# Performance work log

Hardware: AMD Instinct MI355X
Metric: run time of the kernel (lower is better)

The kernel has to match this reference:

```python
import jax, jax.numpy as jnp
import numpy as np

N_GLIMPSES = 3
GS = 64          # glimpse_size
IN_C = 3         # input_channels
B, H, W = 64, 512, 512


def get_glimpses(image, loc):
    """Multi-scale glimpse extraction (tf.image.extract_glimpse, centered+normalized)
    followed by antialiased bicubic resize to GS x GS, concatenated on channels."""
    b, h, w, c = image.shape
    max_size = GS * 2 ** (N_GLIMPSES - 1)
    padded = jnp.pad(image, ((0, 0), (max_size, max_size), (max_size, max_size), (0, 0)))
    hp, wp = h + 2 * max_size, w + 2 * max_size
    # normalized+centered offsets: (-1,-1)=upper-left, (1,1)=lower-right of padded image
    center = (loc + 1.0) * 0.5 * jnp.array([hp, wp], dtype=jnp.float32)  # (y, x) per batch
    glimpses = []
    for i in range(N_GLIMPSES):
        s = GS * 2 ** i  # current crop size (python int, static)
        tl = jnp.round(center - 0.5 * s).astype(jnp.int32)
        tl = jnp.clip(tl, 0, jnp.array([hp - s, wp - s], dtype=jnp.int32))

        def slice_one(img, yx):
            return jax.lax.dynamic_slice(img, (yx[0], yx[1], 0), (s, s, c))

        g = jax.vmap(slice_one)(padded, tl)                      # [B, s, s, C]
        g = jax.image.resize(g, (b, GS, GS, c), method='cubic')  # antialiased bicubic
        glimpses.append(g)
    return jnp.concatenate(glimpses, axis=-1)  # [B, GS, GS, N_GLIMPSES*C]


def setup_inputs() -> dict:
    key = jax.random.key(0)
    ks = jax.random.split(key, 10)
    image = jax.random.uniform(ks[0], (B, H, W, IN_C), dtype=jnp.float32)
    loc = jax.random.uniform(ks[1], (B, 2), dtype=jnp.float32, minval=-1.0, maxval=1.0)
    cg = N_GLIMPSES * IN_C
    # conv1_g: full-kernel (GS x GS) valid conv -> 1x1x128
    Wg = jax.random.normal(ks[2], (GS, GS, cg, 128), dtype=jnp.float32) * (1.0 / np.sqrt(GS * GS * cg))
    bg = jnp.zeros((128,), jnp.float32)
    # conv1_l: 1x1 conv on loc [B,1,1,2]
    Wl = jax.random.normal(ks[3], (2, 128), dtype=jnp.float32) * (1.0 / np.sqrt(2.0))
    bl = jnp.zeros((128,), jnp.float32)
    # out: 1x1 conv 128 -> 256
    Wo = jax.random.normal(ks[4], (128, 256), dtype=jnp.float32) * (1.0 / np.sqrt(128.0))
    bo = jnp.zeros((256,), jnp.float32)
    return {"image": image, "loc": loc, "Wg": Wg, "bg": bg, "Wl": Wl, "bl": bl, "Wo": Wo, "bo": bo}


def reference(image, loc, Wg, bg, Wl, bl, Wo, bo):
    glimpses = get_glimpses(image, loc)  # [B, GS, GS, N_GLIMPSES*IN_C]
    # conv1_g with kernel == glimpse size and VALID padding == dense contraction over hwc
    x1 = jax.nn.relu(jnp.einsum('bhwc,hwck->bk', glimpses, Wg) + bg)  # [B,128]
    x2 = jax.nn.relu(loc @ Wl + bl)                                   # [B,128]
    out = jax.nn.relu((x1 + x2) @ Wo + bo)                            # [B,256]
    return out
```

## Files before the change

kernel.cpp:

```cpp
#include <hip/hip_runtime.h>

#define IMG_H 512
#define IMG_W 512
#define PAD   256
#define HP    1024
#define BATCH 64
#define KTOT  36864
#define KTILE 144
#define KB    16
#define NTILES 256

__device__ __forceinline__ float keys_cubic(float x) {
  if (x >= 2.0f) return 0.0f;
  if (x >= 1.0f) return ((-0.5f * x + 2.5f) * x - 4.0f) * x + 2.0f;
  return ((1.5f * x - 2.5f) * x) * x + 1.0f;
}

__device__ __forceinline__ int iclamp(int v, int lo, int hi) {
  return min(max(v, lo), hi);
}

__global__ __launch_bounds__(256) void glimpse_kernel(
    const float* __restrict__ img, const float* __restrict__ loc,
    float* __restrict__ G) {
  __shared__ float tmp1[384];
  __shared__ float tmp2[768];
  const int y   = blockIdx.x & 63;
  const int b   = blockIdx.x >> 6;
  const int tid = threadIdx.x;

  const float cy = (loc[2 * b] + 1.0f) * 0.5f * 1024.0f;
  const float cx = (loc[2 * b + 1] + 1.0f) * 0.5f * 1024.0f;
  const int tly0 = iclamp((int)rintf(cy - 32.0f), 0, HP - 64);
  const int tlx0 = iclamp((int)rintf(cx - 32.0f), 0, HP - 64);
  const int tly1 = iclamp((int)rintf(cy - 64.0f), 0, HP - 128);
  const int tlx1 = iclamp((int)rintf(cx - 64.0f), 0, HP - 128);
  const int tly2 = iclamp((int)rintf(cy - 128.0f), 0, HP - 256);
  const int tlx2 = iclamp((int)rintf(cx - 128.0f), 0, HP - 256);
  const float* imb  = img + (size_t)b * (IMG_H * IMG_W * 3);
  float*       Grow = G + ((size_t)b * 64 + y) * (64 * 9);

  if (tid < 192) {
    int x = tid / 3, c = tid - 3 * (tid / 3);
    int py = tly0 + y - PAD, px = tlx0 + x - PAD;
    float v = 0.0f;
    if ((unsigned)py < (unsigned)IMG_H && (unsigned)px < (unsigned)IMG_W)
      v = imb[(py * IMG_W + px) * 3 + c];
    Grow[x * 9 + c] = v;
  }

  float wy1[8];
  int iy0_1;
  {
    float sy = ((float)y + 0.5f) * 2.0f - 0.5f;
    iy0_1 = (int)ceilf(sy - 4.0f);
    float ws = 0.0f;
#pragma unroll
    for (int t = 0; t < 8; ++t) {
      int i = iy0_1 + t;
      float w = (i >= 0 && i < 128) ? keys_cubic(fabsf(sy - (float)i) * 0.5f) : 0.0f;
      wy1[t] = w;
      ws += w;
    }
    float wi = 1.0f / ws;
#pragma unroll
    for (int t = 0; t < 8; ++t) wy1[t] *= wi;
  }
  float wy2[16];
  int iy0_2;
  {
    float sy = ((float)y + 0.5f) * 4.0f - 0.5f;
    iy0_2 = (int)ceilf(sy - 8.0f);
    float ws = 0.0f;
#pragma unroll
    for (int t = 0; t < 16; ++t) {
      int i = iy0_2 + t;
      float w = (i >= 0 && i < 256) ? keys_cubic(fabsf(sy - (float)i) * 0.25f) : 0.0f;
      wy2[t] = w;
      ws += w;
    }
    float wi = 1.0f / ws;
#pragma unroll
    for (int t = 0; t < 16; ++t) wy2[t] *= wi;
  }

  for (int e = tid; e < 384; e += 256) {
    int x = e / 3, c = e - 3 * (e / 3);
    int px = tlx1 - PAD + x;
    float a = 0.0f;
    if ((unsigned)px < (unsigned)IMG_W) {
      const float* colp = imb + (px * 3 + c);
#pragma unroll
      for (int t = 0; t < 8; ++t) {
        int py = tly1 + iy0_1 + t - PAD;
        if ((unsigned)py < (unsigned)IMG_H)
          a = fmaf(wy1[t], colp[py * (IMG_W * 3)], a);
      }
    }
    tmp1[e] = a;
  }
  for (int e = tid; e < 768; e += 256) {
    int x = e / 3, c = e - 3 * (e / 3);
    int px = tlx2 - PAD + x;
    float a = 0.0f;
    if ((unsigned)px < (unsigned)IMG_W) {
      const float* colp = imb + (px * 3 + c);
#pragma unroll
      for (int t = 0; t < 16; ++t) {
        int py = tly2 + iy0_2 + t - PAD;
        if ((unsigned)py < (unsigned)IMG_H)
          a = fmaf(wy2[t], colp[py * (IMG_W * 3)], a);
      }
    }
    tmp2[e] = a;
  }
  __syncthreads();

  for (int o = tid; o < 384; o += 256) {
    int oo = (o >= 192) ? o - 192 : o;
    int xo = oo / 3, c = oo - 3 * xo;
    if (o < 192) {
      float sx  = ((float)xo + 0.5f) * 2.0f - 0.5f;
      int   ix0 = (int)ceilf(sx - 4.0f);
      float a = 0.0f, wsx = 0.0f;
#pragma unroll
      for (int t = 0; t < 8; ++t) {
        int i = ix0 + t;
        if (i >= 0 && i < 128) {
          float w = keys_cubic(fabsf(sx - (float)i) * 0.5f);
          wsx += w;
          a = fmaf(w, tmp1[i * 3 + c], a);
        }
      }
      Grow[xo * 9 + 3 + c] = a / wsx;
    } else {
      float sx  = ((float)xo + 0.5f) * 4.0f - 0.5f;
      int   ix0 = (int)ceilf(sx - 8.0f);
      float a = 0.0f, wsx = 0.0f;
#pragma unroll
      for (int t = 0; t < 16; ++t) {
        int i = ix0 + t;
        if (i >= 0 && i < 256) {
          float w = keys_cubic(fabsf(sx - (float)i) * 0.25f);
          wsx += w;
          a = fmaf(w, tmp2[i * 3 + c], a);
        }
      }
      Grow[xo * 9 + 6 + c] = a / wsx;
    }
  }
}

__global__ __launch_bounds__(256) void gemm_kernel(
    const float* __restrict__ G, const float* __restrict__ Wg,
    float* __restrict__ partials) {
  const int tile = blockIdx.x;
  const int tid  = threadIdx.x;
  const int tn   = tid & 15;
  const int tm   = tid >> 4;
  __shared__ float Gs[2][KB][64];
  __shared__ float Ws[2][KB][128];

  const int gb = tid >> 2;
  const int gj = (tid & 3) * 4;
  const int wr = tid >> 4;
  const int wc = (tid & 15) * 8;
  const size_t gbase = (size_t)gb * KTOT + (size_t)tile * KTILE + gj;
  const size_t wbase = ((size_t)tile * KTILE + wr) * 128 + wc;

  float4 g4 = *(const float4*)(G + gbase);
  float4 wa = *(const float4*)(Wg + wbase);
  float4 wb = *(const float4*)(Wg + wbase + 4);

  float acc[4][8];
#pragma unroll
  for (int mi = 0; mi < 4; ++mi)
#pragma unroll
    for (int ni = 0; ni < 8; ++ni) acc[mi][ni] = 0.0f;

  constexpr int NCHUNK = KTILE / KB;
#pragma unroll
  for (int chunk = 0; chunk < NCHUNK; ++chunk) {
    const int buf = chunk & 1;
    Gs[buf][gj + 0][gb] = g4.x;
    Gs[buf][gj + 1][gb] = g4.y;
    Gs[buf][gj + 2][gb] = g4.z;
    Gs[buf][gj + 3][gb] = g4.w;
    *(float4*)&Ws[buf][wr][wc]     = wa;
    *(float4*)&Ws[buf][wr][wc + 4] = wb;
    __syncthreads();
    if (chunk + 1 < NCHUNK) {
      g4 = *(const float4*)(G + gbase + (chunk + 1) * KB);
      wa = *(const float4*)(Wg + wbase + (size_t)(chunk + 1) * KB * 128);
      wb = *(const float4*)(Wg + wbase + (size_t)(chunk + 1) * KB * 128 + 4);
    }
#pragma unroll
    for (int j = 0; j < KB; ++j) {
      float4 gv = *(const float4*)&Gs[buf][j][tm * 4];
      float4 w0 = *(const float4*)&Ws[buf][j][tn * 8];
      float4 w1 = *(const float4*)&Ws[buf][j][tn * 8 + 4];
      float gm[4] = {gv.x, gv.y, gv.z, gv.w};
      float wn[8] = {w0.x, w0.y, w0.z, w0.w, w1.x, w1.y, w1.z, w1.w};
#pragma unroll
      for (int mi = 0; mi < 4; ++mi)
#pragma unroll
        for (int ni = 0; ni < 8; ++ni)
          acc[mi][ni] = fmaf(gm[mi], wn[ni], acc[mi][ni]);
    }
  }

#pragma unroll
  for (int mi = 0; mi < 4; ++mi) {
    int m = tm * 4 + mi;
    float* dst = partials + ((size_t)m * NTILES + tile) * 128 + tn * 8;
    *(float4*)dst       = make_float4(acc[mi][0], acc[mi][1], acc[mi][2], acc[mi][3]);
    *(float4*)(dst + 4) = make_float4(acc[mi][4], acc[mi][5], acc[mi][6], acc[mi][7]);
  }
}

__global__ __launch_bounds__(256) void finalize_kernel(
    const float* __restrict__ partials, const float* __restrict__ loc,
    const float* __restrict__ bg, const float* __restrict__ Wl,
    const float* __restrict__ bl, const float* __restrict__ Wo,
    const float* __restrict__ bo, float* __restrict__ out) {
  const int b   = blockIdx.x;
  const int tid = threadIdx.x;

  const float4* base = (const float4*)(partials + (size_t)b * NTILES * 128);
  float4 acc = make_float4(0.f, 0.f, 0.f, 0.f);
#pragma unroll 8
  for (int i = 0; i < 32; ++i) {
    float4 v = base[(size_t)i * 256 + tid];
    acc.x += v.x; acc.y += v.y; acc.z += v.z; acc.w += v.w;
  }

  __shared__ float red[8][128];
  __shared__ float h[128];
  {
    float* r = &red[tid >> 5][(tid & 31) * 4];
    r[0] = acc.x; r[1] = acc.y; r[2] = acc.z; r[3] = acc.w;
  }
  __syncthreads();
  if (tid < 128) {
    float ss = 0.0f;
#pragma unroll
    for (int g = 0; g < 8; ++g) ss += red[g][tid];
    float x1 = fmaxf(ss + bg[tid], 0.0f);
    float x2 = fmaxf(fmaf(loc[2 * b], Wl[tid],
                          fmaf(loc[2 * b + 1], Wl[128 + tid], bl[tid])),
                     0.0f);
    h[tid] = x1 + x2;
  }
  __syncthreads();
  {
    int n = tid;
    float a = bo[n];
#pragma unroll 8
    for (int kk = 0; kk < 128; ++kk) a = fmaf(h[kk], Wo[kk * 256 + n], a);
    out[(size_t)b * 256 + n] = fmaxf(a, 0.0f);
  }
}

extern "C" void kernel_launch(void* const* d_in, const int* in_sizes, int n_in,
                              void* d_out, int out_size, void* d_ws, size_t ws_size,
                              hipStream_t stream) {
  const float* img = (const float*)d_in[0];
  const float* loc = (const float*)d_in[1];
  const float* Wg  = (const float*)d_in[2];
  const float* bg  = (const float*)d_in[3];
  const float* Wl  = (const float*)d_in[4];
  const float* bl  = (const float*)d_in[5];
  const float* Wo  = (const float*)d_in[6];
  const float* bo  = (const float*)d_in[7];
  float* out = (float*)d_out;

  float* ws = (float*)d_ws;
  float* G        = ws;
  float* partials = ws + 2359296;

  glimpse_kernel<<<BATCH * 64, 256, 0, stream>>>(img, loc, G);
  gemm_kernel<<<NTILES, 256, 0, stream>>>(G, Wg, partials);
  finalize_kernel<<<BATCH, 256, 0, stream>>>(partials, loc, bg, Wl, bl, Wo, bo, out);
}
```

Before: 318.8 us.

## Rewrite glimpse and GEMM kernels with bf16 MFMA and precomputed cubic weights

The glimpse kernel now handles 16-row strips per block, split by scale. Each block reads image rows once and accumulates vertical taps in registers, using compile-time normalized bicubic weights in place of per-pixel weight evaluation. The glimpse buffer is stored in bf16, and the GEMM now uses bf16 MFMA 16x16x32 instructions with Wg converted on the fly, which cuts memory traffic and ALU work. The trade-off is reduced precision (bf16 operands) and uncoalesced strided Wg loads in the GEMM.

```diff
diff --git a/kernel.cpp b/kernel.cpp
--- a/kernel.cpp
+++ b/kernel.cpp
@@ -1,4 +1,5 @@
 #include <hip/hip_runtime.h>
+#include <hip/hip_bf16.h>
 
 #define IMG_H 512
 #define IMG_W 512
@@ -6,216 +7,284 @@
 #define HP    1024
 #define BATCH 64
 #define KTOT  36864
-#define KTILE 144
-#define KB    16
-#define NTILES 256
-
-__device__ __forceinline__ float keys_cubic(float x) {
-  if (x >= 2.0f) return 0.0f;
-  if (x >= 1.0f) return ((-0.5f * x + 2.5f) * x - 4.0f) * x + 2.0f;
-  return ((1.5f * x - 2.5f) * x) * x + 1.0f;
-}
-
-__device__ __forceinline__ int iclamp(int v, int lo, int hi) {
-  return min(max(v, lo), hi);
+#define KTILE 192
+#define NTILES 192
+
+typedef __attribute__((ext_vector_type(8))) short short8;
+typedef __attribute__((ext_vector_type(4))) float f32x4;
+
+constexpr float keysc(float a) {
+  return a >= 2.0f ? 0.0f
+       : a >= 1.0f ? ((-0.5f * a + 2.5f) * a - 4.0f) * a + 2.0f
+       : (1.5f * a - 2.5f) * a * a + 1.0f;
+}
+constexpr float fabsc(float x) { return x < 0.f ? -x : x; }
+constexpr float K2c(int t) { return keysc(fabsc(7.5f - (float)t) * 0.25f); }
+constexpr float K1c(int t) { return keysc(fabsc(3.5f - (float)t) * 0.5f); }
+constexpr float C2 = K2c(0)+K2c(1)+K2c(2)+K2c(3)+K2c(4)+K2c(5)+K2c(6)+K2c(7)
+                    +K2c(8)+K2c(9)+K2c(10)+K2c(11)+K2c(12)+K2c(13)+K2c(14)+K2c(15);
+constexpr float C1 = K1c(0)+K1c(1)+K1c(2)+K1c(3)+K1c(4)+K1c(5)+K1c(6)+K1c(7);
+__device__ constexpr float KN2[16] = {
+  K2c(0)/C2, K2c(1)/C2, K2c(2)/C2, K2c(3)/C2, K2c(4)/C2, K2c(5)/C2, K2c(6)/C2, K2c(7)/C2,
+  K2c(8)/C2, K2c(9)/C2, K2c(10)/C2, K2c(11)/C2, K2c(12)/C2, K2c(13)/C2, K2c(14)/C2, K2c(15)/C2};
+__device__ constexpr float KN1[8] = {
+  K1c(0)/C1, K1c(1)/C1, K1c(2)/C1, K1c(3)/C1, K1c(4)/C1, K1c(5)/C1, K1c(6)/C1, K1c(7)/C1};
+
+__device__ __forceinline__ float enorm2(int o) {
+  if (o >= 2 && o <= 61) return 1.0f;
+  float s = 0.f;
+#pragma unroll
+  for (int t = 0; t < 16; ++t) { int i = 4 * o - 6 + t; if ((unsigned)i < 256u) s += KN2[t]; }
+  return 1.0f / s;
+}
+__device__ __forceinline__ float enorm1(int o) {
+  if (o >= 2 && o <= 61) return 1.0f;
+  float s = 0.f;
+#pragma unroll
+  for (int t = 0; t < 8; ++t) { int i = 2 * o - 3 + t; if ((unsigned)i < 128u) s += KN1[t]; }
+  return 1.0f / s;
+}
+
+__device__ __forceinline__ int iclamp(int v, int lo, int hi) { return min(max(v, lo), hi); }
+__device__ __forceinline__ unsigned short f2bits(float f) {
+  __hip_bfloat16 h = __float2bfloat16(f);
+  unsigned short s;
+  __builtin_memcpy(&s, &h, 2);
+  return s;
 }
 
 __global__ __launch_bounds__(256) void glimpse_kernel(
     const float* __restrict__ img, const float* __restrict__ loc,
-    float* __restrict__ G) {
-  __shared__ float tmp1[384];
-  __shared__ float tmp2[768];
-  const int y   = blockIdx.x & 63;
-  const int b   = blockIdx.x >> 6;
+    unsigned short* __restrict__ G) {
+  __shared__ __align__(16) float smem[16 * 768 + 16];
+  float* tmp = smem;
+  float* vn  = smem + 16 * 768;
+
+  const int blk = blockIdx.x;
+  const int b   = blk / 12;
+  const int r12 = blk - 12 * b;
   const int tid = threadIdx.x;
 
   const float cy = (loc[2 * b] + 1.0f) * 0.5f * 1024.0f;
   const float cx = (loc[2 * b + 1] + 1.0f) * 0.5f * 1024.0f;
-  const int tly0 = iclamp((int)rintf(cy - 32.0f), 0, HP - 64);
-  const int tlx0 = iclamp((int)rintf(cx - 32.0f), 0, HP - 64);
-  const int tly1 = iclamp((int)rintf(cy - 64.0f), 0, HP - 128);
-  const int tlx1 = iclamp((int)rintf(cx - 64.0f), 0, HP - 128);
-  const int tly2 = iclamp((int)rintf(cy - 128.0f), 0, HP - 256);
-  const int tlx2 = iclamp((int)rintf(cx - 128.0f), 0, HP - 256);
-  const float* imb  = img + (size_t)b * (IMG_H * IMG_W * 3);
-  float*       Grow = G + ((size_t)b * 64 + y) * (64 * 9);
-
-  if (tid < 192) {
-    int x = tid / 3, c = tid - 3 * (tid / 3);
-    int py = tly0 + y - PAD, px = tlx0 + x - PAD;
-    float v = 0.0f;
-    if ((unsigned)py < (unsigned)IMG_H && (unsigned)px < (unsigned)IMG_W)
-      v = imb[(py * IMG_W + px) * 3 + c];
-    Grow[x * 9 + c] = v;
-  }
-
-  float wy1[8];
-  int iy0_1;
+  const float* imb = img + (size_t)b * (IMG_H * IMG_W * 3);
+
+  if (r12 >= 8) {
+    const int y0 = 16 * (r12 - 8);
+    const int tly0 = iclamp((int)rintf(cy - 32.0f), 0, HP - 64);
+    const int tlx0 = iclamp((int)rintf(cx - 32.0f), 0, HP - 64);
+#pragma unroll
+    for (int p = 0; p < 12; ++p) {
+      int oi = tid + 256 * p;
+      int yl = oi / 192, rem = oi - 192 * yl, x = rem / 3, c = rem - 3 * x;
+      int py = tly0 + y0 + yl - PAD, px = tlx0 + x - PAD;
+      float v = 0.0f;
+      if ((unsigned)py < (unsigned)IMG_H && (unsigned)px < (unsigned)IMG_W)
+        v = imb[(py * IMG_W + px) * 3 + c];
+      G[(((size_t)b * 64 + y0 + yl) * 64 + x) * 9 + c] = f2bits(v);
+    }
+    return;
+  }
+
+  if (r12 < 4) {
+    const int y0 = 16 * r12;
+    const int tly = iclamp((int)rintf(cy - 128.0f), 0, HP - 256);
+    const int tlx = iclamp((int)rintf(cx - 128.0f), 0, HP - 256);
+    const int cb = (tlx - PAD) * 3;
+    const int xA = tid / 3, xB = (tid + 256) / 3, xC = (tid + 512) / 3;
+    const bool mA = (unsigned)(tlx - PAD + xA) < (unsigned)IMG_W;
+    const bool mB = (unsigned)(tlx - PAD + xB) < (unsigned)IMG_W;
+    const bool mC = (unsigned)(tlx - PAD + xC) < (unsigned)IMG_W;
+    float a0[16], a1[16], a2[16];
+#pragma unroll
+    for (int i = 0; i < 16; ++i) { a0[i] = 0.f; a1[i] = 0.f; a2[i] = 0.f; }
+    const int rbase = 4 * y0 - 6;
+#pragma unroll
+    for (int k = 0; k < 76; ++k) {
+      const int r = rbase + k;
+      const int py = tly - PAD + r;
+      if ((unsigned)r < 256u && (unsigned)py < (unsigned)IMG_H) {
+        const float* rp = imb + (size_t)py * (IMG_W * 3) + cb;
+        float v0 = mA ? rp[tid] : 0.f;
+        float v1 = mB ? rp[tid + 256] : 0.f;
+        float v2 = mC ? rp[tid + 512] : 0.f;
+#pragma unroll
+        for (int d = 0; d < 4; ++d) {
+          const int yl = (k >> 2) - d;
+          const int t  = (k & 3) + 4 * d;
+          if (yl >= 0 && yl < 16) {
+            const float w = KN2[t];
+            a0[yl] = fmaf(w, v0, a0[yl]);
+            a1[yl] = fmaf(w, v1, a1[yl]);
+            a2[yl] = fmaf(w, v2, a2[yl]);
+          }
+        }
+      }
+    }
+#pragma unroll
+    for (int yl = 0; yl < 16; ++yl) {
+      tmp[yl * 768 + tid]       = a0[yl];
+      tmp[yl * 768 + tid + 256] = a1[yl];
+      tmp[yl * 768 + tid + 512] = a2[yl];
+    }
+    if (tid < 16) vn[tid] = enorm2(y0 + tid);
+    __syncthreads();
+#pragma unroll
+    for (int p = 0; p < 12; ++p) {
+      int oi = tid + 256 * p;
+      int yl = oi / 192, rem = oi - 192 * yl, xo = rem / 3, c = rem - 3 * xo;
+      const float* trow = tmp + yl * 768 + c;
+      const int i0 = 4 * xo - 6;
+      float a = 0.f;
+      if (xo >= 2 && xo <= 61) {
+#pragma unroll
+        for (int t = 0; t < 16; ++t) a = fmaf(KN2[t], trow[(i0 + t) * 3], a);
+      } else {
+#pragma unroll
+        for (int t = 0; t < 16; ++t) {
+          int i = i0 + t;
+          if ((unsigned)i < 256u) a = fmaf(KN2[t], trow[i * 3], a);
+        }
+      }
+      a *= enorm2(xo) * vn[yl];
+      G[(((size_t)b * 64 + y0 + yl) * 64 + xo) * 9 + 6 + c] = f2bits(a);
+    }
+    return;
+  }
+
   {
-    float sy = ((float)y + 0.5f) * 2.0f - 0.5f;
-    iy0_1 = (int)ceilf(sy - 4.0f);
-    float ws = 0.0f;
-#pragma unroll
-    for (int t = 0; t < 8; ++t) {
-      int i = iy0_1 + t;
-      float w = (i >= 0 && i < 128) ? keys_cubic(fabsf(sy - (float)i) * 0.5f) : 0.0f;
-      wy1[t] = w;
-      ws += w;
-    }
-    float wi = 1.0f / ws;
-#pragma unroll
-    for (int t = 0; t < 8; ++t) wy1[t] *= wi;
-  }
-  float wy2[16];
-  int iy0_2;
+    const int y0 = 16 * (r12 - 4);
+    const int tly = iclamp((int)rintf(cy - 64.0f), 0, HP - 128);
+    const int tlx = iclamp((int)rintf(cx - 64.0f), 0, HP - 128);
+    const int cb = (tlx - PAD) * 3;
+    float a0[16], a1[16];
+#pragma unroll
+    for (int i = 0; i < 16; ++i) { a0[i] = 0.f; a1[i] = 0.f; }
+    const int e0 = 2 * tid, e1 = 2 * tid + 1;
+    const bool act = tid < 192;
+    const bool mA = act && ((unsigned)(tlx - PAD + e0 / 3) < (unsigned)IMG_W);
+    const bool mB = act && ((unsigned)(tlx - PAD + e1 / 3) < (unsigned)IMG_W);
+    const int rbase = 2 * y0 - 3;
+#pragma unroll
+    for (int k = 0; k < 38; ++k) {
+      const int r = rbase + k;
+      const int py = tly - PAD + r;
+      if ((unsigned)r < 128u && (unsigned)py < (unsigned)IMG_H) {
+        const float* rp = imb + (size_t)py * (IMG_W * 3) + cb;
+        float v0 = mA ? rp[e0] : 0.f;
+        float v1 = mB ? rp[e1] : 0.f;
+#pragma unroll
+        for (int d = 0; d < 4; ++d) {
+          const int yl = (k >> 1) - d;
+          const int t  = (k & 1) + 2 * d;
+          if (yl >= 0 && yl < 16) {
+            const float w = KN1[t];
+            a0[yl] = fmaf(w, v0, a0[yl]);
+            a1[yl] = fmaf(w, v1, a1[yl]);
+          }
+        }
+      }
+    }
+    if (act) {
+#pragma unroll
+      for (int yl = 0; yl < 16; ++yl) {
+        tmp[yl * 384 + e0] = a0[yl];
+        tmp[yl * 384 + e1] = a1[yl];
+      }
+    }
+    if (tid < 16) vn[tid] = enorm1(y0 + tid);
+    __syncthreads();
+#pragma unroll
+    for (int p = 0; p < 12; ++p) {
+      int oi = tid + 256 * p;
+      int yl = oi / 192, rem = oi - 192 * yl, xo = rem / 3, c = rem - 3 * xo;
+      const float* trow = tmp + yl * 384 + c;
+      const int i0 = 2 * xo - 3;
+      float a = 0.f;
+      if (xo >= 2 && xo <= 61) {
+#pragma unroll
+        for (int t = 0; t < 8; ++t) a = fmaf(KN1[t], trow[(i0 + t) * 3], a);
+      } else {
+#pragma unroll
+        for (int t = 0; t < 8; ++t) {
+          int i = i0 + t;
+          if ((unsigned)i < 128u) a = fmaf(KN1[t], trow[i * 3], a);
+        }
+      }
+      a *= enorm1(xo) * vn[yl];
+      G[(((size_t)b * 64 + y0 + yl) * 64 + xo) * 9 + 3 + c] = f2bits(a);
+    }
+  }
+}
+
+__global__ __launch_bounds__(256) void gemm_kernel(
+    const unsigned short* __restrict__ G, const float* __restrict__ Wg,
+    float* __restrict__ partials) {
+  __shared__ __align__(16) unsigned short Gs[64 * 200];
+  const int tid  = threadIdx.x;
+  const int tile = blockIdx.x;
+  const int kt   = tile * KTILE;
+
   {
-    float sy = ((float)y + 0.5f) * 4.0f - 0.5f;
-    iy0_2 = (int)ceilf(sy - 8.0f);
-    float ws = 0.0f;
-#pragma unroll
-    for (int t = 0; t < 16; ++t) {
-      int i = iy0_2 + t;
-      float w = (i >= 0 && i < 256) ? keys_cubic(fabsf(sy - (float)i) * 0.25f) : 0.0f;
-      wy2[t] = w;
-      ws += w;
-    }
-    float wi = 1.0f / ws;
-#pragma unroll
-    for (int t = 0; t < 16; ++t) wy2[t] *= wi;
-  }
-
-  for (int e = tid; e < 384; e += 256) {
-    int x = e / 3, c = e - 3 * (e / 3);
-    int px = tlx1 - PAD + x;
-    float a = 0.0f;
-    if ((unsigned)px < (unsigned)IMG_W) {
-      const float* colp = imb + (px * 3 + c);
-#pragma unroll
-      for (int t = 0; t < 8; ++t) {
-        int py = tly1 + iy0_1 + t - PAD;
-        if ((unsigned)py < (unsigned)IMG_H)
-          a = fmaf(wy1[t], colp[py * (IMG_W * 3)], a);
-      }
-    }
-    tmp1[e] = a;
-  }
-  for (int e = tid; e < 768; e += 256) {
-    int x = e / 3, c = e - 3 * (e / 3);
-    int px = tlx2 - PAD + x;
-    float a = 0.0f;
-    if ((unsigned)px < (unsigned)IMG_W) {
-      const float* colp = imb + (px * 3 + c);
-#pragma unroll
-      for (int t = 0; t < 16; ++t) {
-        int py = tly2 + iy0_2 + t - PAD;
-        if ((unsigned)py < (unsigned)IMG_H)
-          a = fmaf(wy2[t], colp[py * (IMG_W * 3)], a);
-      }
-    }
-    tmp2[e] = a;
+    const int m = tid >> 2, i = tid & 3;
+    const unsigned short* src = G + (size_t)m * KTOT + kt;
+    unsigned short* dst = Gs + m * 200;
+#pragma unroll
+    for (int p = 0; p < 6; ++p) {
+      const int o8 = (i + 4 * p) * 8;
+      *(float4*)(dst + o8) = *(const float4*)(src + o8);
+    }
   }
   __syncthreads();
 
-  for (int o = tid; o < 384; o += 256) {
-    int oo = (o >= 192) ? o - 192 : o;
-    int xo = oo / 3, c = oo - 3 * xo;
-    if (o < 192) {
-      float sx  = ((float)xo + 0.5f) * 2.0f - 0.5f;
-      int   ix0 = (int)ceilf(sx - 4.0f);
-      float a = 0.0f, wsx = 0.0f;
-#pragma unroll
-      for (int t = 0; t < 8; ++t) {
-        int i = ix0 + t;
-        if (i >= 0 && i < 128) {
-          float w = keys_cubic(fabsf(sx - (float)i) * 0.5f);
-          wsx += w;
-          a = fmaf(w, tmp1[i * 3 + c], a);
-        }
-      }
-      Grow[xo * 9 + 3 + c] = a / wsx;
-    } else {
-      float sx  = ((float)xo + 0.5f) * 4.0f - 0.5f;
-      int   ix0 = (int)ceilf(sx - 8.0f);
-      float a = 0.0f, wsx = 0.0f;
-#pragma unroll
-      for (int t = 0; t < 16; ++t) {
-        int i = ix0 + t;
-        if (i >= 0 && i < 256) {
-          float w = keys_cubic(fabsf(sx - (float)i) * 0.25f);
-          wsx += w;
-          a = fmaf(w, tmp2[i * 3 + c], a);
-        }
-      }
-      Grow[xo * 9 + 6 + c] = a / wsx;
-    }
-  }
-}
-
-__global__ __launch_bounds__(256) void gemm_kernel(
-    const float* __restrict__ G, const float* __restrict__ Wg,
-    float* __restrict__ partials) {
-  const int tile = blockIdx.x;
-  const int tid  = threadIdx.x;
-  const int tn   = tid & 15;
-  const int tm   = tid >> 4;
-  __shared__ float Gs[2][KB][64];
-  __shared__ float Ws[2][KB][128];
-
-  const int gb = tid >> 2;
-  const int gj = (tid & 3) * 4;
-  const int wr = tid >> 4;
-  const int wc = (tid & 15) * 8;
-  const size_t gbase = (size_t)gb * KTOT + (size_t)tile * KTILE + gj;
-  const size_t wbase = ((size_t)tile * KTILE + wr) * 128 + wc;
-
-  float4 g4 = *(const float4*)(G + gbase);
-  float4 wa = *(const float4*)(Wg + wbase);
-  float4 wb = *(const float4*)(Wg + wbase + 4);
-
-  float acc[4][8];
-#pragma unroll
-  for (int mi = 0; mi < 4; ++mi)
-#pragma unroll
-    for (int ni = 0; ni < 8; ++ni) acc[mi][ni] = 0.0f;
-
-  constexpr int NCHUNK = KTILE / KB;
-#pragma unroll
-  for (int chunk = 0; chunk < NCHUNK; ++chunk) {
-    const int buf = chunk & 1;
-    Gs[buf][gj + 0][gb] = g4.x;
-    Gs[buf][gj + 1][gb] = g4.y;
-    Gs[buf][gj + 2][gb] = g4.z;
-    Gs[buf][gj + 3][gb] = g4.w;
-    *(float4*)&Ws[buf][wr][wc]     = wa;
-    *(float4*)&Ws[buf][wr][wc + 4] = wb;
-    __syncthreads();
-    if (chunk + 1 < NCHUNK) {
-      g4 = *(const float4*)(G + gbase + (chunk + 1) * KB);
-      wa = *(const float4*)(Wg + wbase + (size_t)(chunk + 1) * KB * 128);
-      wb = *(const float4*)(Wg + wbase + (size_t)(chunk + 1) * KB * 128 + 4);
-    }
-#pragma unroll
-    for (int j = 0; j < KB; ++j) {
-      float4 gv = *(const float4*)&Gs[buf][j][tm * 4];
-      float4 w0 = *(const float4*)&Ws[buf][j][tn * 8];
-      float4 w1 = *(const float4*)&Ws[buf][j][tn * 8 + 4];
-      float gm[4] = {gv.x, gv.y, gv.z, gv.w};
-      float wn[8] = {w0.x, w0.y, w0.z, w0.w, w1.x, w1.y, w1.z, w1.w};
-#pragma unroll
-      for (int mi = 0; mi < 4; ++mi)
-#pragma unroll
-        for (int ni = 0; ni < 8; ++ni)
-          acc[mi][ni] = fmaf(gm[mi], wn[ni], acc[mi][ni]);
-    }
-  }
-
-#pragma unroll
-  for (int mi = 0; mi < 4; ++mi) {
-    int m = tm * 4 + mi;
-    float* dst = partials + ((size_t)m * NTILES + tile) * 128 + tn * 8;
-    *(float4*)dst       = make_float4(acc[mi][0], acc[mi][1], acc[mi][2], acc[mi][3]);
-    *(float4*)(dst + 4) = make_float4(acc[mi][4], acc[mi][5], acc[mi][6], acc[mi][7]);
-  }
+  const int lane = tid & 63;
+  const int wv   = tid >> 6;
+  const int ln   = lane & 15;
+  const int q    = lane >> 4;
+  const int nb   = wv * 32 + ln;
+
+  f32x4 acc[4][2];
+#pragma unroll
+  for (int mt = 0; mt < 4; ++mt)
+#pragma unroll
+    for (int nt = 0; nt < 2; ++nt) {
+      acc[mt][nt][0] = 0.f; acc[mt][nt][1] = 0.f;
+      acc[mt][nt][2] = 0.f; acc[mt][nt][3] = 0.f;
+    }
+
+#pragma unroll
+  for (int s = 0; s < 6; ++s) {
+    short8 af[4];
+#pragma unroll
+    for (int mt = 0; mt < 4; ++mt)
+      af[mt] = *(const short8*)(Gs + (mt * 16 + ln) * 200 + s * 32 + q * 8);
+    short8 bf[2];
+#pragma unroll
+    for (int nt = 0; nt < 2; ++nt) {
+      const float* wp = Wg + (size_t)(kt + s * 32 + q * 8) * 128 + nb + nt * 16;
+      short8 v;
+#pragma unroll
+      for (int j = 0; j < 8; ++j) v[j] = (short)f2bits(wp[j * 128]);
+      bf[nt] = v;
+    }
+#pragma unroll
+    for (int mt = 0; mt < 4; ++mt)
+#pragma unroll
+      for (int nt = 0; nt < 2; ++nt)
+        acc[mt][nt] = __builtin_amdgcn_mfma_f32_16x16x32_bf16(
+            af[mt], bf[nt], acc[mt][nt], 0, 0, 0);
+  }
+
+#pragma unroll
+  for (int mt = 0; mt < 4; ++mt)
+#pragma unroll
+    for (int nt = 0; nt < 2; ++nt)
+#pragma unroll
+      for (int i = 0; i < 4; ++i) {
+        const int row = mt * 16 + q * 4 + i;
+        const int col = nb + nt * 16;
+        partials[((size_t)row * NTILES + tile) * 128 + col] = acc[mt][nt][i];
+      }
 }
 
 __global__ __launch_bounds__(256) void finalize_kernel(
@@ -228,8 +297,8 @@
 
   const float4* base = (const float4*)(partials + (size_t)b * NTILES * 128);
   float4 acc = make_float4(0.f, 0.f, 0.f, 0.f);
-#pragma unroll 8
-  for (int i = 0; i < 32; ++i) {
+#pragma unroll 6
+  for (int i = 0; i < 24; ++i) {
     float4 v = base[(size_t)i * 256 + tid];
     acc.x += v.x; acc.y += v.y; acc.z += v.z; acc.w += v.w;
   }
@@ -253,7 +322,7 @@
   }
   __syncthreads();
   {
-    int n = tid;
+    const int n = tid;
     float a = bo[n];
 #pragma unroll 8
     for (int kk = 0; kk < 128; ++kk) a = fmaf(h[kk], Wo[kk * 256 + n], a);
@@ -274,11 +343,11 @@
   const float* bo  = (const float*)d_in[7];
   float* out = (float*)d_out;
 
-  float* ws = (float*)d_ws;
-  float* G        = ws;
-  float* partials = ws + 2359296;
-
-  glimpse_kernel<<<BATCH * 64, 256, 0, stream>>>(img, loc, G);
+  char* ws = (char*)d_ws;
+  unsigned short* G = (unsigned short*)ws;
+  float* partials   = (float*)(ws + 2359296 * 2);
+
+  glimpse_kernel<<<BATCH * 12, 256, 0, stream>>>(img, loc, G);
   gemm_kernel<<<NTILES, 256, 0, stream>>>(G, Wg, partials);
   finalize_kernel<<<BATCH, 256, 0, stream>>>(partials, loc, bg, Wl, bl, Wo, bo, out);
 }
```

Result: slower. 359.6 us (+12.8%).
